# Kernel tuning notes

Hardware: AMD Instinct MI355X
Metric: run time of the kernel (lower is better)

Reference implementation:

```python
import jax, jax.numpy as jnp
import numpy as np

N = 50000      # nodes
E = 400000     # edges per hop
IN = 256       # in_channels
H = 4          # heads
C = 64         # out_channels per head
NEG = 0.2      # leaky relu negative slope


def setup_inputs() -> dict:
    key = jax.random.key(0)
    ks = jax.random.split(key, 10)
    x = jax.random.normal(ks[0], (N, IN), dtype=jnp.float32)
    edge_index1 = jax.random.randint(ks[1], (2, E), 0, N, dtype=jnp.int32)
    edge_index2 = jax.random.randint(ks[2], (2, E), 0, N, dtype=jnp.int32)
    s = 0.05
    Wl0 = jax.random.normal(ks[3], (IN, H * C), dtype=jnp.float32) * s
    Wr0 = jax.random.normal(ks[4], (IN, H * C), dtype=jnp.float32) * s
    att0 = jax.random.normal(ks[5], (H, C), dtype=jnp.float32) * s
    Wl1 = jax.random.normal(ks[6], (IN, H * C), dtype=jnp.float32) * s
    Wr1 = jax.random.normal(ks[7], (IN, H * C), dtype=jnp.float32) * s
    att1 = jax.random.normal(ks[8], (H, C), dtype=jnp.float32) * s
    return {"x": x, "Wl0": Wl0, "Wr0": Wr0, "att0": att0,
            "Wl1": Wl1, "Wr1": Wr1, "att1": att1,
            "edge_index1": edge_index1, "edge_index2": edge_index2}


def _gatv2_hop(x, Wl, Wr, att, src, dst):
    """One GATv2Conv hop (bias=False, residual=False, eval-mode dropout, concat=False)."""
    n = x.shape[0]
    xl = (x @ Wl).reshape(n, H, C)   # source-side projection
    xr = (x @ Wr).reshape(n, H, C)   # target-side projection
    # edge-wise GATv2 score: a^T leaky_relu(x_l[j] + x_r[i])
    m = jax.nn.leaky_relu(xl[src] + xr[dst], NEG)            # [E, H, C]
    e = jnp.einsum('ehc,hc->eh', m, att)                     # [E, H]
    # segment softmax over incoming edges of each destination node
    e_max = jax.lax.stop_gradient(
        jax.ops.segment_max(e, dst, num_segments=n))         # [N, H]
    ex = jnp.exp(e - e_max[dst])
    denom = jax.ops.segment_sum(ex, dst, num_segments=n)     # [N, H]
    alpha = ex / (denom[dst] + 1e-16)                        # [E, H]
    msg = xl[src] * alpha[:, :, None]                        # [E, H, C]
    out = jax.ops.segment_sum(msg, dst, num_segments=n)      # [N, H, C]
    return out.mean(axis=1)                                  # concat=False -> mean heads


def reference(x, Wl0, Wr0, att0, Wl1, Wr1, att1, edge_index1, edge_index2):
    n = x.shape[0]
    # hop 0: add_self_loops=True
    loop = jnp.arange(n, dtype=edge_index1.dtype)
    src0 = jnp.concatenate([edge_index1[0], loop])
    dst0 = jnp.concatenate([edge_index1[1], loop])
    out = _gatv2_hop(x, Wl0, Wr0, att0, src0, dst0)
    # hop 1: no self loops, scaled by 1/(k+1) = 1/2
    out = out + _gatv2_hop(x, Wl1, Wr1, att1, edge_index2[0], edge_index2[1]) / 2.0
    return out
```

## Files before the change

### kernel.cpp

```cpp
#include <hip/hip_runtime.h>

typedef unsigned int uint;
typedef unsigned short ushort;

typedef __bf16 bf16x8 __attribute__((ext_vector_type(8)));
typedef float f32x4 __attribute__((ext_vector_type(4)));
typedef float f32x2 __attribute__((ext_vector_type(2)));

#define CAP 48
#define RSTR 136

__device__ __forceinline__ float bf2f(ushort u) {
    return __uint_as_float(((uint)u) << 16);
}
__device__ __forceinline__ ushort f2bf(float f) {
    uint u = __float_as_uint(f);
    u += 0x7fffu + ((u >> 16) & 1u);
    return (ushort)(u >> 16);
}
__device__ __forceinline__ void load_lds16(const ushort* g, ushort* l) {
    __builtin_amdgcn_global_load_lds(
        (const __attribute__((address_space(1))) void*)g,
        (__attribute__((address_space(3))) void*)l, 16, 0, 0);
}
__device__ __forceinline__ f32x2 up2(uint u) {
    f32x2 r;
    r.x = __uint_as_float(u << 16);
    r.y = __uint_as_float(u & 0xffff0000u);
    return r;
}

template<int CTRL>
__device__ __forceinline__ float dppadd(float p) {
    int t = __builtin_amdgcn_update_dpp(0, __float_as_int(p), CTRL, 0xf, 0xf, true);
    return p + __int_as_float(t);
}

__global__ __launch_bounds__(256) void prep(
    const float* __restrict__ X, ushort* __restrict__ Xb, int Nrows, int Mpad,
    const float* __restrict__ Wl0, const float* __restrict__ Wr0,
    const float* __restrict__ Wl1, const float* __restrict__ Wr1,
    ushort* __restrict__ Wt)
{
    const int BX = Mpad / 8;
    int blk = blockIdx.x;
    if (blk < BX) {
        int i = blk * 256 + threadIdx.x;
        int base = i * 8;
        int row = base >> 8;
        ushort o[8];
        if (row < Nrows) {
            float4 v0 = *(const float4*)(X + base);
            float4 v1 = *(const float4*)(X + base + 4);
            o[0] = f2bf(v0.x); o[1] = f2bf(v0.y); o[2] = f2bf(v0.z); o[3] = f2bf(v0.w);
            o[4] = f2bf(v1.x); o[5] = f2bf(v1.y); o[6] = f2bf(v1.z); o[7] = f2bf(v1.w);
        } else {
#pragma unroll
            for (int j = 0; j < 8; j++) o[j] = 0;
        }
        *(uint4*)(Xb + base) = *(const uint4*)o;
        return;
    }
    blk -= BX;
    int n = blk;
    int k = threadIdx.x;
    const float* W = (n < 256) ? Wl0 : (n < 512) ? Wr0 : (n < 768) ? Wl1 : Wr1;
    Wt[n * 256 + k] = f2bf(W[k * 256 + (n & 255)]);
}

__global__ __launch_bounds__(256, 2) void gemm_scatter(
    const ushort* __restrict__ Xb,
    const ushort* __restrict__ Wt,
    ushort* __restrict__ XP,
    int Nrows, int GB, int cshift,
    const int* __restrict__ ei1, const int* __restrict__ ei2,
    int* __restrict__ cnt0, int* __restrict__ srcs0,
    int* __restrict__ cnt1, int* __restrict__ srcs1,
    int E1, int E2)
{
    int blk = blockIdx.x;
    if (blk >= GB) {
        int e = (blk - GB) * 256 + threadIdx.x;
        if (e < E1) {
            int d = ei1[E1 + e];
            int pos = atomicAdd(&cnt0[d], 1);
            if (pos < CAP) srcs0[(size_t)d * CAP + pos] = ei1[e];
        } else if (e < E1 + E2) {
            int e2 = e - E1;
            int d = ei2[E2 + e2];
            int pos = atomicAdd(&cnt1[d], 1);
            if (pos < CAP) srcs1[(size_t)d * CAP + pos] = ei2[e2];
        }
        return;
    }

    __shared__ ushort SH[2 * 128 * 64];
    ushort* As = SH;
    ushort* Bs = SH + 128 * 64;

    const int tid = threadIdx.x;
    const int w = tid >> 6, l = tid & 63;
    const int wm = w & 1, wn = w >> 1;
    const int m0 = (blk >> cshift) * 128;
    const int n0g = (blk & ((1 << cshift) - 1)) * 128;

    f32x4 acc[4][4];
#pragma unroll
    for (int i = 0; i < 4; i++)
#pragma unroll
        for (int j = 0; j < 4; j++) acc[i][j] = (f32x4)(0.f);

    const int fr = l & 15, fq = l >> 4;
    int a_off[2][4], b_off[2][4];
#pragma unroll
    for (int g = 0; g < 2; g++)
#pragma unroll
        for (int t = 0; t < 4; t++) {
            int c = g * 4 + fq;
            int rA = wm * 64 + t * 16 + fr;
            a_off[g][t] = (rA * 8 + ((c + rA) & 7)) * 8;
            int rB = wn * 64 + t * 16 + fr;
            b_off[g][t] = (rB * 8 + ((c + rB) & 7)) * 8;
        }

    for (int k0 = 0; k0 < 256; k0 += 64) {
        __syncthreads();
#pragma unroll
        for (int rnd = 0; rnd < 4; rnd++) {
            int slot = rnd * 256 + tid;
            int row = slot >> 3;
            int c = ((slot & 7) - row) & 7;
            load_lds16(Xb + (size_t)(m0 + row) * 256 + k0 + c * 8,
                       &As[(rnd * 256 + w * 64) * 8]);
            load_lds16(Wt + (size_t)(n0g + row) * 256 + k0 + c * 8,
                       &Bs[(rnd * 256 + w * 64) * 8]);
        }
        __syncthreads();

#pragma unroll
        for (int g = 0; g < 2; g++) {
            bf16x8 a[4], b[4];
#pragma unroll
            for (int t = 0; t < 4; t++) {
                a[t] = *(const bf16x8*)(As + a_off[g][t]);
                b[t] = *(const bf16x8*)(Bs + b_off[g][t]);
            }
#pragma unroll
            for (int mi = 0; mi < 4; mi++)
#pragma unroll
                for (int ni = 0; ni < 4; ni++)
                    acc[mi][ni] = __builtin_amdgcn_mfma_f32_16x16x32_bf16(
                        a[mi], b[ni], acc[mi][ni], 0, 0, 0);
        }
    }

    ushort* OUT = XP + (size_t)(n0g >> 8) * ((size_t)Nrows * 256);
    const int colbase = n0g & 255;
    const int cb = wn * 64 + fr;
#pragma unroll
    for (int r = 0; r < 2; r++) {
        __syncthreads();
#pragma unroll
        for (int mm = 0; mm < 2; mm++) {
            int mi = 2 * r + mm;
            int brb = (wm * 32 + mm * 16 + fq * 4) * RSTR + cb;
#pragma unroll
            for (int reg = 0; reg < 4; reg++)
#pragma unroll
                for (int ni = 0; ni < 4; ni++)
                    SH[brb + reg * RSTR + ni * 16] = f2bf(acc[mi][ni][reg]);
        }
        __syncthreads();
        int br = tid >> 2;
        int grow = m0 + (br >> 5) * 64 + (2 * r + ((br >> 4) & 1)) * 16 + (br & 15);
        bool ok = (grow < Nrows);
        int cc = (tid & 3) * 8;
#pragma unroll
        for (int q = 0; q < 4; q++) {
            uint4 v = *(const uint4*)(SH + br * RSTR + cc + q * 32);
            if (ok) *(uint4*)(OUT + (size_t)grow * 256 + colbase + cc + q * 32) = v;
        }
    }
}

__device__ __forceinline__ uint4 pair_load(const ushort* __restrict__ XL, int sv,
                                           int e, int cp, uint hl, uint sub16)
{
    int eA = (e     < cp) ? e     : cp;
    int eB = (e + 1 < cp) ? e + 1 : cp;
    uint sA = (uint)__builtin_amdgcn_readlane(sv, eA) * 512u;
    uint sB = (uint)__builtin_amdgcn_readlane(sv, eB) * 512u;
    uint off = sA + hl * (sB - sA) + sub16;
    return *(const uint4*)((const char*)XL + off);
}

__device__ __forceinline__ void eaccp(uint4 raw, int deadB, uint hl,
    const f32x2* __restrict__ xr2, const f32x2* __restrict__ av2,
    f32x2* __restrict__ acc, float& den)
{
    f32x2 xv[4];
    xv[0] = up2(raw.x);
    xv[1] = up2(raw.y);
    xv[2] = up2(raw.z);
    xv[3] = up2(raw.w);
    f32x2 p2 = (f32x2)(0.f);
#pragma unroll
    for (int k = 0; k < 4; k++) {
        f32x2 t = xv[k] + xr2[k];
        f32x2 u = t * 0.2f;
        t.x = fmaxf(t.x, u.x);
        t.y = fmaxf(t.y, u.y);
        p2 += t * av2[k];
    }
    float p = p2.x + p2.y;
    p = dppadd<0xB1>(p);
    p = dppadd<0x4E>(p);
    p = dppadd<0x141>(p);
    float pe = __expf(p);
    if (deadB & (int)hl) pe = 0.f;
    den += pe;
#pragma unroll
    for (int k = 0; k < 4; k++) acc[k] += xv[k] * pe;
}

__device__ __forceinline__ void gat_hop(
    const ushort* __restrict__ XL, const ushort* __restrict__ XR,
    const float* __restrict__ att, const int* __restrict__ cnt,
    const int* __restrict__ srcs, int self, int d, int lane,
    uint hl, uint sub, uint sub16,
    f32x2* __restrict__ acc, float& den)
{
    uint4 xrr = *(const uint4*)((const char*)XR + (uint)d * 512u + sub16);
    f32x2 xr2[4];
    xr2[0] = up2(xrr.x);
    xr2[1] = up2(xrr.y);
    xr2[2] = up2(xrr.z);
    xr2[3] = up2(xrr.w);
    float4 a0 = *(const float4*)(att + sub * 8);
    float4 a1 = *(const float4*)(att + sub * 8 + 4);
    f32x2 av2[4];
    av2[0].x = a0.x; av2[0].y = a0.y;
    av2[1].x = a0.z; av2[1].y = a0.w;
    av2[2].x = a1.x; av2[2].y = a1.y;
    av2[3].x = a1.z; av2[3].y = a1.w;

#pragma unroll
    for (int k = 0; k < 4; k++) acc[k] = (f32x2)(0.f);
    den = 0.f;

    int m = __builtin_amdgcn_readfirstlane(cnt[d]);
    if (m > CAP) m = CAP;
    const int mt = m + self;
    if (mt <= 0) return;

    int idx = lane - self;
    int mm1 = (m > 0) ? (m - 1) : 0;
    int slot = idx < 0 ? 0 : (idx > mm1 ? mm1 : idx);
    int sv = srcs[(size_t)d * CAP + slot];
    if (self && lane == 0) sv = d;

    const int cp = mt - 1;
    uint4 pf0 = pair_load(XL, sv, 0, cp, hl, sub16);
    uint4 pf1 = pair_load(XL, sv, 2, cp, hl, sub16);
    for (int i = 0; i < mt; i += 4) {
        uint4 c0 = pf0, c1 = pf1;
        pf0 = pair_load(XL, sv, i + 4, cp, hl, sub16);
        pf1 = pair_load(XL, sv, i + 6, cp, hl, sub16);
        eaccp(c0, (i + 1 >= mt) ? 1 : 0, hl, xr2, av2, acc, den);
        if (i + 2 < mt)
            eaccp(c1, (i + 3 >= mt) ? 1 : 0, hl, xr2, av2, acc, den);
    }
}

__global__ __launch_bounds__(256) void gat_fused(
    const ushort* __restrict__ XL0, const ushort* __restrict__ XR0,
    const float* __restrict__ att0,
    const int* __restrict__ cnt0, const int* __restrict__ srcs0,
    int self0, float scale0,
    const ushort* __restrict__ XL1, const ushort* __restrict__ XR1,
    const float* __restrict__ att1,
    const int* __restrict__ cnt1, const int* __restrict__ srcs1,
    float scale1,
    const float* __restrict__ base, float* __restrict__ outp, int N)
{
    int d = blockIdx.x * 4 + (threadIdx.x >> 6);
    if (d >= N) return;
    int lane = threadIdx.x & 63;
    uint hl = (uint)(lane >> 5);
    uint sub = (uint)(lane & 31);
    uint sub16 = sub * 16u;

    f32x2 acc0[4];
    float den0;
    gat_hop(XL0, XR0, att0, cnt0, srcs0, self0, d, lane, hl, sub, sub16, acc0, den0);

    float v[8];
    den0 += __shfl_xor(den0, 32);
    float s0 = scale0 / (den0 + 1e-16f);
    if (cnt1) {
        f32x2 acc1[4];
        float den1;
        gat_hop(XL1, XR1, att1, cnt1, srcs1, 0, d, lane, hl, sub, sub16, acc1, den1);
        den1 += __shfl_xor(den1, 32);
        float s1 = scale1 / (den1 + 1e-16f);
#pragma unroll
        for (int k = 0; k < 4; k++) {
            v[2 * k]     = acc0[k].x * s0 + acc1[k].x * s1;
            v[2 * k + 1] = acc0[k].y * s0 + acc1[k].y * s1;
        }
    } else {
#pragma unroll
        for (int k = 0; k < 4; k++) {
            v[2 * k]     = acc0[k].x * s0;
            v[2 * k + 1] = acc0[k].y * s0;
        }
    }
#pragma unroll
    for (int j = 0; j < 8; j++) {
        v[j] += __shfl_xor(v[j], 8);
        v[j] += __shfl_xor(v[j], 16);
        v[j] += __shfl_xor(v[j], 32);
    }
    if (lane < 8) {
        float* dst = outp + (size_t)d * 64 + lane * 8;
        float4 w0 = {v[0], v[1], v[2], v[3]};
        float4 w1 = {v[4], v[5], v[6], v[7]};
        if (base) {
            float4 b0 = *(const float4*)(base + (size_t)d * 64 + lane * 8);
            float4 b1 = *(const float4*)(base + (size_t)d * 64 + lane * 8 + 4);
            w0.x += b0.x; w0.y += b0.y; w0.z += b0.z; w0.w += b0.w;
            w1.x += b1.x; w1.y += b1.y; w1.z += b1.z; w1.w += b1.w;
        }
        *(float4*)dst = w0;
        *(float4*)(dst + 4) = w1;
    }
}

extern "C" void kernel_launch(void* const* d_in, const int* in_sizes, int n_in,
                              void* d_out, int out_size, void* d_ws, size_t ws_size,
                              hipStream_t stream)
{
    const float* x    = (const float*)d_in[0];
    const float* Wl0  = (const float*)d_in[1];
    const float* Wr0  = (const float*)d_in[2];
    const float* att0 = (const float*)d_in[3];
    const float* Wl1  = (const float*)d_in[4];
    const float* Wr1  = (const float*)d_in[5];
    const float* att1 = (const float*)d_in[6];
    const int* ei1 = (const int*)d_in[7];
    const int* ei2 = (const int*)d_in[8];

    const int N  = in_sizes[0] / 256;
    const int E1 = in_sizes[7] / 2;
    const int E2 = in_sizes[8] / 2;
    const int Mpad = ((N + 127) / 128) * 128;
    const size_t NB = (size_t)N * 256;

    char* ws = (char*)d_ws;
    size_t off = 0;
    ushort* Xb  = (ushort*)(ws + off); off += (size_t)Mpad * 256 * sizeof(ushort);
    ushort* Wt  = (ushort*)(ws + off); off += (size_t)1024 * 256 * sizeof(ushort);
    int* cnt0   = (int*)(ws + off);    off += (size_t)N * sizeof(int);
    int* cnt1   = (int*)(ws + off);    off += (size_t)N * sizeof(int);
    int* srcs0  = (int*)(ws + off);    off += (size_t)N * CAP * sizeof(int);
    int* srcs1  = (int*)(ws + off);    off += (size_t)N * CAP * sizeof(int);
    ushort* XP  = (ushort*)(ws + off);
    size_t need_mega = off + 4 * NB * sizeof(ushort);
    const bool mega = (ws_size >= need_mega);
    float* outf = (float*)d_out;

    hipMemsetAsync(cnt0, 0, 2 * (size_t)N * sizeof(int), stream);

    const int BX = Mpad / 8;
    prep<<<BX + 1024, 256, 0, stream>>>(x, Xb, N, Mpad, Wl0, Wr0, Wl1, Wr1, Wt);

    const int SB = (E1 + E2 + 255) / 256;
    int aggblk = (N + 3) / 4;
    if (mega) {
        int GB = 8 * (Mpad / 128);
        gemm_scatter<<<GB + SB, 256, 0, stream>>>(
            Xb, Wt, XP, N, GB, 3,
            ei1, ei2, cnt0, srcs0, cnt1, srcs1, E1, E2);
        gat_fused<<<aggblk, 256, 0, stream>>>(
            XP, XP + NB, att0, cnt0, srcs0, 1, 0.25f,
            XP + 2 * NB, XP + 3 * NB, att1, cnt1, srcs1, 0.125f,
            nullptr, outf, N);
    } else {
        int GB = 4 * (Mpad / 128);
        gemm_scatter<<<GB + SB, 256, 0, stream>>>(
            Xb, Wt, XP, N, GB, 2,
            ei1, ei2, cnt0, srcs0, cnt1, srcs1, E1, E2);
        gat_fused<<<aggblk, 256, 0, stream>>>(
            XP, XP + NB, att0, cnt0, srcs0, 1, 0.25f,
            nullptr, nullptr, nullptr, nullptr, nullptr, 0.f,
            nullptr, outf, N);
        gemm_scatter<<<GB, 256, 0, stream>>>(
            Xb, Wt + 512 * 256, XP, N, GB, 2,
            nullptr, nullptr, cnt0, srcs0, cnt1, srcs1, 0, 0);
        gat_fused<<<aggblk, 256, 0, stream>>>(
            XP, XP + NB, att1, cnt1, srcs1, 0, 0.125f,
            nullptr, nullptr, nullptr, nullptr, nullptr, 0.f,
            outf, outf, N);
    }
}
```

Measured before the change: 280.5 us.

## Move edge scatter into prep kernel and remap GEMM blocks per XCD

Result: faster. 256.7 us (-8.5%).

```diff
diff --git a/kernel.cpp b/kernel.cpp
--- a/kernel.cpp
+++ b/kernel.cpp
@@ -36,14 +36,33 @@
     return p + __int_as_float(t);
 }
 
-__global__ __launch_bounds__(256) void prep(
+__global__ __launch_bounds__(256) void prep_scatter(
     const float* __restrict__ X, ushort* __restrict__ Xb, int Nrows, int Mpad,
     const float* __restrict__ Wl0, const float* __restrict__ Wr0,
     const float* __restrict__ Wl1, const float* __restrict__ Wr1,
-    ushort* __restrict__ Wt)
-{
+    ushort* __restrict__ Wt,
+    const int* __restrict__ ei1, const int* __restrict__ ei2,
+    int* __restrict__ cnt0, int* __restrict__ srcs0,
+    int* __restrict__ cnt1, int* __restrict__ srcs1,
+    int E1, int E2, int SB)
+{
+    int blk = blockIdx.x;
+    if (blk < SB) {
+        int e = blk * 256 + threadIdx.x;
+        if (e < E1) {
+            int d = ei1[E1 + e];
+            int pos = atomicAdd(&cnt0[d], 1);
+            if (pos < CAP) srcs0[(size_t)d * CAP + pos] = ei1[e];
+        } else if (e < E1 + E2) {
+            int e2 = e - E1;
+            int d = ei2[E2 + e2];
+            int pos = atomicAdd(&cnt1[d], 1);
+            if (pos < CAP) srcs1[(size_t)d * CAP + pos] = ei2[e2];
+        }
+        return;
+    }
+    blk -= SB;
     const int BX = Mpad / 8;
-    int blk = blockIdx.x;
     if (blk < BX) {
         int i = blk * 256 + threadIdx.x;
         int base = i * 8;
@@ -68,31 +87,19 @@
     Wt[n * 256 + k] = f2bf(W[k * 256 + (n & 255)]);
 }
 
-__global__ __launch_bounds__(256, 2) void gemm_scatter(
+__global__ __launch_bounds__(256, 4) void gemm_mfma(
     const ushort* __restrict__ Xb,
     const ushort* __restrict__ Wt,
     ushort* __restrict__ XP,
-    int Nrows, int GB, int cshift,
-    const int* __restrict__ ei1, const int* __restrict__ ei2,
-    int* __restrict__ cnt0, int* __restrict__ srcs0,
-    int* __restrict__ cnt1, int* __restrict__ srcs1,
-    int E1, int E2)
-{
-    int blk = blockIdx.x;
-    if (blk >= GB) {
-        int e = (blk - GB) * 256 + threadIdx.x;
-        if (e < E1) {
-            int d = ei1[E1 + e];
-            int pos = atomicAdd(&cnt0[d], 1);
-            if (pos < CAP) srcs0[(size_t)d * CAP + pos] = ei1[e];
-        } else if (e < E1 + E2) {
-            int e2 = e - E1;
-            int d = ei2[E2 + e2];
-            int pos = atomicAdd(&cnt1[d], 1);
-            if (pos < CAP) srcs1[(size_t)d * CAP + pos] = ei2[e2];
-        }
-        return;
-    }
+    int Nrows, int Pp, int nbshift)
+{
+    int b = blockIdx.x;
+    int xcd = b & 7;
+    int i = b >> 3;
+    int p = xcd * Pp + (i >> nbshift);
+    int j = i & ((1 << nbshift) - 1);
+    const int m0 = p * 128;
+    const int n0g = j * 128;
 
     __shared__ ushort SH[2 * 128 * 64];
     ushort* As = SH;
@@ -101,14 +108,12 @@
     const int tid = threadIdx.x;
     const int w = tid >> 6, l = tid & 63;
     const int wm = w & 1, wn = w >> 1;
-    const int m0 = (blk >> cshift) * 128;
-    const int n0g = (blk & ((1 << cshift) - 1)) * 128;
 
     f32x4 acc[4][4];
 #pragma unroll
-    for (int i = 0; i < 4; i++)
-#pragma unroll
-        for (int j = 0; j < 4; j++) acc[i][j] = (f32x4)(0.f);
+    for (int ii = 0; ii < 4; ii++)
+#pragma unroll
+        for (int jj = 0; jj < 4; jj++) acc[ii][jj] = (f32x4)(0.f);
 
     const int fr = l & 15, fq = l >> 4;
     int a_off[2][4], b_off[2][4];
@@ -139,18 +144,18 @@
 
 #pragma unroll
         for (int g = 0; g < 2; g++) {
-            bf16x8 a[4], b[4];
+            bf16x8 a[4], bfr[4];
 #pragma unroll
             for (int t = 0; t < 4; t++) {
-                a[t] = *(const bf16x8*)(As + a_off[g][t]);
-                b[t] = *(const bf16x8*)(Bs + b_off[g][t]);
+                a[t]   = *(const bf16x8*)(As + a_off[g][t]);
+                bfr[t] = *(const bf16x8*)(Bs + b_off[g][t]);
             }
 #pragma unroll
             for (int mi = 0; mi < 4; mi++)
 #pragma unroll
                 for (int ni = 0; ni < 4; ni++)
                     acc[mi][ni] = __builtin_amdgcn_mfma_f32_16x16x32_bf16(
-                        a[mi], b[ni], acc[mi][ni], 0, 0, 0);
+                        a[mi], bfr[ni], acc[mi][ni], 0, 0, 0);
         }
     }
 
@@ -353,7 +358,9 @@
     const int N  = in_sizes[0] / 256;
     const int E1 = in_sizes[7] / 2;
     const int E2 = in_sizes[8] / 2;
-    const int Mpad = ((N + 127) / 128) * 128;
+    const int Mpad = ((N + 1023) / 1024) * 1024;
+    const int P  = Mpad / 128;
+    const int Pp = P / 8;
     const size_t NB = (size_t)N * 256;
 
     char* ws = (char*)d_ws;
@@ -372,31 +379,25 @@
     hipMemsetAsync(cnt0, 0, 2 * (size_t)N * sizeof(int), stream);
 
     const int BX = Mpad / 8;
-    prep<<<BX + 1024, 256, 0, stream>>>(x, Xb, N, Mpad, Wl0, Wr0, Wl1, Wr1, Wt);
-
     const int SB = (E1 + E2 + 255) / 256;
+    prep_scatter<<<SB + BX + 1024, 256, 0, stream>>>(
+        x, Xb, N, Mpad, Wl0, Wr0, Wl1, Wr1, Wt,
+        ei1, ei2, cnt0, srcs0, cnt1, srcs1, E1, E2, SB);
+
     int aggblk = (N + 3) / 4;
     if (mega) {
-        int GB = 8 * (Mpad / 128);
-        gemm_scatter<<<GB + SB, 256, 0, stream>>>(
-            Xb, Wt, XP, N, GB, 3,
-            ei1, ei2, cnt0, srcs0, cnt1, srcs1, E1, E2);
+        gemm_mfma<<<P * 8, 256, 0, stream>>>(Xb, Wt, XP, N, Pp, 3);
         gat_fused<<<aggblk, 256, 0, stream>>>(
             XP, XP + NB, att0, cnt0, srcs0, 1, 0.25f,
             XP + 2 * NB, XP + 3 * NB, att1, cnt1, srcs1, 0.125f,
             nullptr, outf, N);
     } else {
-        int GB = 4 * (Mpad / 128);
-        gemm_scatter<<<GB + SB, 256, 0, stream>>>(
-            Xb, Wt, XP, N, GB, 2,
-            ei1, ei2, cnt0, srcs0, cnt1, srcs1, E1, E2);
+        gemm_mfma<<<P * 4, 256, 0, stream>>>(Xb, Wt, XP, N, Pp, 2);
         gat_fused<<<aggblk, 256, 0, stream>>>(
             XP, XP + NB, att0, cnt0, srcs0, 1, 0.25f,
             nullptr, nullptr, nullptr, nullptr, nullptr, 0.f,
             nullptr, outf, N);
-        gemm_scatter<<<GB, 256, 0, stream>>>(
-            Xb, Wt + 512 * 256, XP, N, GB, 2,
-            nullptr, nullptr, cnt0, srcs0, cnt1, srcs1, 0, 0);
+        gemm_mfma<<<P * 4, 256, 0, stream>>>(Xb, Wt + 512 * 256, XP, N, Pp, 2);
         gat_fused<<<aggblk, 256, 0, stream>>>(
             XP, XP + NB, att1, cnt1, srcs1, 0, 0.125f,
             nullptr, nullptr, nullptr, nullptr, nullptr, 0.f,
```
